# Optimization experiments

Hardware: AMD Instinct MI355X
Metric: run time of the kernel (lower is better)

The kernel has to match this reference:

```python
import jax, jax.numpy as jnp
import numpy as np
from jax import lax

B, T, I, H, O = 64, 512, 256, 1024, 1


def setup_inputs() -> dict:
    key = jax.random.key(0)
    ks = jax.random.split(key, 7)
    s_ih = 1.0 / np.sqrt(H)
    return {
        "x": jax.random.normal(ks[0], (B, T, I), dtype=jnp.float32),
        "W_ih": jax.random.uniform(ks[1], (4 * H, I), minval=-s_ih, maxval=s_ih, dtype=jnp.float32),
        "W_hh": jax.random.uniform(ks[2], (4 * H, H), minval=-s_ih, maxval=s_ih, dtype=jnp.float32),
        "b_ih": jax.random.uniform(ks[3], (4 * H,), minval=-s_ih, maxval=s_ih, dtype=jnp.float32),
        "b_hh": jax.random.uniform(ks[4], (4 * H,), minval=-s_ih, maxval=s_ih, dtype=jnp.float32),
        "fc_W": jax.random.uniform(ks[5], (O, H), minval=-s_ih, maxval=s_ih, dtype=jnp.float32),
        "fc_b": jax.random.uniform(ks[6], (O,), minval=-s_ih, maxval=s_ih, dtype=jnp.float32),
    }


def reference(x, W_ih, W_hh, b_ih, b_hh, fc_W, fc_b):
    Bd, Td, _ = x.shape
    Hd = W_hh.shape[1]
    # Precompute input projections for all timesteps: [T, B, 4H]
    x_proj = jnp.einsum('bti,gi->tbg', x, W_ih) + b_ih + b_hh

    def step(carry, xt):
        h, c = carry
        gates = xt + h @ W_hh.T  # [B, 4H]
        i_g, f_g, g_g, o_g = jnp.split(gates, 4, axis=-1)  # PyTorch order i,f,g,o
        i_g = jax.nn.sigmoid(i_g)
        f_g = jax.nn.sigmoid(f_g)
        g_g = jnp.tanh(g_g)
        o_g = jax.nn.sigmoid(o_g)
        c_new = f_g * c + i_g * g_g
        h_new = o_g * jnp.tanh(c_new)
        return (h_new, c_new), None

    h0 = jnp.zeros((Bd, Hd), dtype=x.dtype)
    c0 = jnp.zeros((Bd, Hd), dtype=x.dtype)
    (h_last, _), _ = lax.scan(step, (h0, c0), x_proj)
    out = jnp.tanh(h_last)          # tanh on last hidden state
    return out @ fc_W.T + fc_b      # [B, O]
```

## Files before the change

kernel.cpp:

```cpp
#include <hip/hip_runtime.h>
#include <hip/hip_bf16.h>


typedef __bf16 bf16_t;
typedef bf16_t b16x8 __attribute__((ext_vector_type(8)));
typedef short  s16x8 __attribute__((ext_vector_type(8)));
typedef float  f32x4 __attribute__((ext_vector_type(4)));

#define TQ 512
#define IQ 256
#define HQ 1024

union U8 { b16x8 b; s16x8 s; unsigned short u[8]; unsigned long long q[2]; };

__device__ __forceinline__ float bf2f(unsigned short s) {
    return __uint_as_float(((unsigned)s) << 16);
}
__device__ __forceinline__ unsigned short f2bf(float f) {
    unsigned u = __float_as_uint(f);
    u += 0x7fff + ((u >> 16) & 1);
    return (unsigned short)(u >> 16);
}
__device__ __forceinline__ b16x8 cvt84(float4 a, float4 b) {
    U8 r;
    r.u[0] = f2bf(a.x); r.u[1] = f2bf(a.y); r.u[2] = f2bf(a.z); r.u[3] = f2bf(a.w);
    r.u[4] = f2bf(b.x); r.u[5] = f2bf(b.y); r.u[6] = f2bf(b.z); r.u[7] = f2bf(b.w);
    return r.b;
}
__device__ __forceinline__ b16x8 load_h16(const unsigned short* p) {
    U8 r;
    r.q[0] = __hip_atomic_load((const unsigned long long*)p,
                               __ATOMIC_RELAXED, __HIP_MEMORY_SCOPE_AGENT);
    r.q[1] = __hip_atomic_load((const unsigned long long*)(p + 4),
                               __ATOMIC_RELAXED, __HIP_MEMORY_SCOPE_AGENT);
    return r.b;
}
__device__ __forceinline__ float sigm(float x) {
    return 1.f / (1.f + __expf(-x));
}
__device__ __forceinline__ float tanh_f(float v) {
    float x = fminf(fmaxf(v, -15.f), 15.f);
    float e = __expf(2.f * x);
    return (e - 1.f) / (e + 1.f);
}

__launch_bounds__(512, 2)
__global__ void lstm_persist(const float* __restrict__ x,
                             const float* __restrict__ Wih,
                             const float* __restrict__ Whh,
                             const float* __restrict__ bih,
                             const float* __restrict__ bhh,
                             const float* __restrict__ fcW,
                             const float* __restrict__ fcb,
                             float* __restrict__ out,
                             unsigned short* __restrict__ hbuf,
                             unsigned int* __restrict__ bar)
{
    __shared__ float red[8 * 4 * 64 * 4];

    const int tid  = threadIdx.x;
    const int w    = tid >> 6;
    const int lane = tid & 63;
    const int bid  = blockIdx.x;
    const int bg   = bid & 3;
    const int ug   = bid >> 2;

    const int l16  = lane & 15;
    const int quad = lane >> 4;

    b16x8 wih[4];
    b16x8 whh[4][4];
    {
        const int koff = quad * 8;
        #pragma unroll
        for (int g = 0; g < 4; ++g) {
            int row = g * HQ + ug * 16 + l16;
            const float* p = Wih + (size_t)row * IQ + w * 32 + koff;
            float4 a = *(const float4*)p;
            float4 b = *(const float4*)(p + 4);
            wih[g] = cvt84(a, b);
            #pragma unroll
            for (int j = 0; j < 4; ++j) {
                int k0 = (w * 4 + j) * 32 + koff;
                const float* q = Whh + (size_t)row * HQ + k0;
                float4 c = *(const float4*)q;
                float4 d = *(const float4*)(q + 4);
                whh[j][g] = cvt84(c, d);
            }
        }
    }

    float c_st[4] = {0.f, 0.f, 0.f, 0.f};
    float bias_r[4];
    if (w == 0) {
        #pragma unroll
        for (int g = 0; g < 4; ++g) {
            int gr = g * HQ + ug * 16 + l16;
            bias_r[g] = bih[gr] + bhh[gr];
        }
    }

    unsigned int* mybar = &bar[bg * 64];

    const float* xbase = x + ((size_t)(bg * 16 + l16) * TQ) * IQ + w * 32 + quad * 8;
    float4 xa = *(const float4*)(xbase);
    float4 xb = *(const float4*)(xbase + 4);

    for (int t = 0; t < TQ; ++t) {
        const int p = t & 1;

        b16x8 ax = cvt84(xa, xb);
        f32x4 acc[4];
        #pragma unroll
        for (int g = 0; g < 4; ++g) {
            f32x4 z = {0.f, 0.f, 0.f, 0.f};
            acc[g] = __builtin_amdgcn_mfma_f32_16x16x32_bf16(ax, wih[g], z, 0, 0, 0);
        }

        if (t && tid == 0) {
            unsigned target = 64u * (unsigned)t;
            while (__hip_atomic_load(mybar, __ATOMIC_RELAXED,
                                     __HIP_MEMORY_SCOPE_AGENT) < target)
                __builtin_amdgcn_s_sleep(1);
        }
        __syncthreads();
        asm volatile("" ::: "memory");

        const unsigned short* hread = hbuf + ((size_t)p * 4 + bg) * (16 * HQ);
        b16x8 ah[4];
        #pragma unroll
        for (int j = 0; j < 4; ++j)
            ah[j] = load_h16(hread + (size_t)l16 * HQ + (w * 4 + j) * 32 + quad * 8);
        #pragma unroll
        for (int j = 0; j < 4; ++j) {
            #pragma unroll
            for (int g = 0; g < 4; ++g)
                acc[g] = __builtin_amdgcn_mfma_f32_16x16x32_bf16(ah[j], whh[j][g], acc[g], 0, 0, 0);
        }

        #pragma unroll
        for (int g = 0; g < 4; ++g)
            *(f32x4*)&red[((w * 4 + g) * 64 + lane) * 4] = acc[g];
        __syncthreads();

        {
            size_t nt = (t + 1 < TQ) ? (size_t)(t + 1) * IQ : (size_t)t * IQ;
            xa = *(const float4*)(xbase + nt);
            xb = *(const float4*)(xbase + nt + 4);
        }

        if (w == 0) {
            f32x4 gv[4];
            #pragma unroll
            for (int g = 0; g < 4; ++g) {
                f32x4 s = *(const f32x4*)&red[((0 * 4 + g) * 64 + lane) * 4];
                #pragma unroll
                for (int ww = 1; ww < 8; ++ww)
                    s += *(const f32x4*)&red[((ww * 4 + g) * 64 + lane) * 4];
                gv[g] = s;
            }
            unsigned short* hw = hbuf + ((size_t)(p ^ 1) * 4 + bg) * (16 * HQ)
                               + (size_t)ug * 16 + l16;
            #pragma unroll
            for (int r = 0; r < 4; ++r) {
                float gi = gv[0][r] + bias_r[0];
                float gf = gv[1][r] + bias_r[1];
                float gg = gv[2][r] + bias_r[2];
                float go = gv[3][r] + bias_r[3];
                float i_s = sigm(gi);
                float f_s = sigm(gf);
                float g_t = tanh_f(gg);
                float o_s = sigm(go);
                float c = f_s * c_st[r] + i_s * g_t;
                c_st[r] = c;
                float h = o_s * tanh_f(c);
                int b = quad * 4 + r;
                __hip_atomic_store(hw + (size_t)b * HQ, f2bf(h),
                                   __ATOMIC_RELAXED, __HIP_MEMORY_SCOPE_AGENT);
            }
            __builtin_amdgcn_s_waitcnt(0);
            if (tid == 0)
                __hip_atomic_fetch_add(mybar, 1u, __ATOMIC_RELAXED,
                                       __HIP_MEMORY_SCOPE_AGENT);
        }
    }

    if (bid < 4) {
        if (tid == 0) {
            unsigned target = 64u * (unsigned)TQ;
            while (__hip_atomic_load(mybar, __ATOMIC_RELAXED,
                                     __HIP_MEMORY_SCOPE_AGENT) < target)
                __builtin_amdgcn_s_sleep(1);
        }
        __syncthreads();
        const unsigned short* hl = hbuf + (size_t)bg * (16 * HQ);
        float fb = fcb[0];
        #pragma unroll
        for (int r = 0; r < 2; ++r) {
            int b = w * 2 + r;
            float s = 0.f;
            #pragma unroll
            for (int j = 0; j < 16; ++j) {
                int u = j * 64 + lane;
                unsigned short hv = __hip_atomic_load(hl + b * HQ + u,
                                                      __ATOMIC_RELAXED,
                                                      __HIP_MEMORY_SCOPE_AGENT);
                s += tanh_f(bf2f(hv)) * fcW[u];
            }
            #pragma unroll
            for (int off = 32; off > 0; off >>= 1)
                s += __shfl_down(s, off);
            if (lane == 0) out[bg * 16 + b] = s + fb;
        }
    }
}

extern "C" void kernel_launch(void* const* d_in, const int* in_sizes, int n_in,
                              void* d_out, int out_size, void* d_ws, size_t ws_size,
                              hipStream_t stream) {
    (void)in_sizes; (void)n_in; (void)out_size; (void)ws_size;
    const float* x   = (const float*)d_in[0];
    const float* Wih = (const float*)d_in[1];
    const float* Whh = (const float*)d_in[2];
    const float* bih = (const float*)d_in[3];
    const float* bhh = (const float*)d_in[4];
    const float* fcW = (const float*)d_in[5];
    const float* fcb = (const float*)d_in[6];
    float* out = (float*)d_out;

    unsigned short* hbuf = (unsigned short*)d_ws;
    unsigned int*   bar  = (unsigned int*)((char*)d_ws + 262144);

    hipMemsetAsync(d_ws, 0, 262144 + 1024, stream);

    void* args[] = { &x, &Wih, &Whh, &bih, &bhh, &fcW, &fcb, &out, &hbuf, &bar };
    hipLaunchCooperativeKernel(reinterpret_cast<void*>(lstm_persist),
                               dim3(256), dim3(512), args, 0, stream);
}
```

Baseline: 2.462 ms.

## Replace atomic counter barrier with per-producer flags polled per wave

```diff
diff --git a/kernel.cpp b/kernel.cpp
--- a/kernel.cpp
+++ b/kernel.cpp
@@ -4,14 +4,13 @@
 
 typedef __bf16 bf16_t;
 typedef bf16_t b16x8 __attribute__((ext_vector_type(8)));
-typedef short  s16x8 __attribute__((ext_vector_type(8)));
 typedef float  f32x4 __attribute__((ext_vector_type(4)));
 
 #define TQ 512
 #define IQ 256
 #define HQ 1024
 
-union U8 { b16x8 b; s16x8 s; unsigned short u[8]; unsigned long long q[2]; };
+union U8 { b16x8 b; unsigned long long q[2]; unsigned short u[8]; };
 
 __device__ __forceinline__ float bf2f(unsigned short s) {
     return __uint_as_float(((unsigned)s) << 16);
@@ -56,7 +55,7 @@
                              unsigned short* __restrict__ hbuf,
                              unsigned int* __restrict__ bar)
 {
-    __shared__ float red[8 * 4 * 64 * 4];
+    __shared__ float red[2 * 8192];
 
     const int tid  = threadIdx.x;
     const int w    = tid >> 6;
@@ -100,7 +99,8 @@
         }
     }
 
-    unsigned int* mybar = &bar[bg * 64];
+    unsigned int* fl = bar + (size_t)bg * 1024;
+    const unsigned int* myfl = fl + (size_t)(w * 8 + (lane & 7)) * 16;
 
     const float* xbase = x + ((size_t)(bg * 16 + l16) * TQ) * IQ + w * 32 + quad * 8;
     float4 xa = *(const float4*)(xbase);
@@ -117,14 +117,14 @@
             acc[g] = __builtin_amdgcn_mfma_f32_16x16x32_bf16(ax, wih[g], z, 0, 0, 0);
         }
 
-        if (t && tid == 0) {
-            unsigned target = 64u * (unsigned)t;
-            while (__hip_atomic_load(mybar, __ATOMIC_RELAXED,
-                                     __HIP_MEMORY_SCOPE_AGENT) < target)
-                __builtin_amdgcn_s_sleep(1);
-        }
-        __syncthreads();
-        asm volatile("" ::: "memory");
+        if (t) {
+            unsigned tv = (unsigned)t;
+            unsigned v = __hip_atomic_load(myfl, __ATOMIC_RELAXED,
+                                           __HIP_MEMORY_SCOPE_AGENT);
+            while (!__all(v >= tv))
+                v = __hip_atomic_load(myfl, __ATOMIC_RELAXED,
+                                      __HIP_MEMORY_SCOPE_AGENT);
+        }
 
         const unsigned short* hread = hbuf + ((size_t)p * 4 + bg) * (16 * HQ);
         b16x8 ah[4];
@@ -138,25 +138,20 @@
                 acc[g] = __builtin_amdgcn_mfma_f32_16x16x32_bf16(ah[j], whh[j][g], acc[g], 0, 0, 0);
         }
 
+        float* rb = &red[p * 8192];
         #pragma unroll
         for (int g = 0; g < 4; ++g)
-            *(f32x4*)&red[((w * 4 + g) * 64 + lane) * 4] = acc[g];
+            *(f32x4*)&rb[((w * 4 + g) * 64 + lane) * 4] = acc[g];
         __syncthreads();
-
-        {
-            size_t nt = (t + 1 < TQ) ? (size_t)(t + 1) * IQ : (size_t)t * IQ;
-            xa = *(const float4*)(xbase + nt);
-            xb = *(const float4*)(xbase + nt + 4);
-        }
 
         if (w == 0) {
             f32x4 gv[4];
             #pragma unroll
             for (int g = 0; g < 4; ++g) {
-                f32x4 s = *(const f32x4*)&red[((0 * 4 + g) * 64 + lane) * 4];
+                f32x4 s = *(const f32x4*)&rb[((0 * 4 + g) * 64 + lane) * 4];
                 #pragma unroll
                 for (int ww = 1; ww < 8; ++ww)
-                    s += *(const f32x4*)&red[((ww * 4 + g) * 64 + lane) * 4];
+                    s += *(const f32x4*)&rb[((ww * 4 + g) * 64 + lane) * 4];
                 gv[g] = s;
             }
             unsigned short* hw = hbuf + ((size_t)(p ^ 1) * 4 + bg) * (16 * HQ)
@@ -178,19 +173,28 @@
                 __hip_atomic_store(hw + (size_t)b * HQ, f2bf(h),
                                    __ATOMIC_RELAXED, __HIP_MEMORY_SCOPE_AGENT);
             }
-            __builtin_amdgcn_s_waitcnt(0);
-            if (tid == 0)
-                __hip_atomic_fetch_add(mybar, 1u, __ATOMIC_RELAXED,
-                                       __HIP_MEMORY_SCOPE_AGENT);
+            asm volatile("s_waitcnt vmcnt(0)" ::: "memory");
+            if (lane == 0)
+                __hip_atomic_store(fl + (size_t)ug * 16, (unsigned)(t + 1),
+                                   __ATOMIC_RELAXED, __HIP_MEMORY_SCOPE_AGENT);
+            size_t nt = (t + 1 < TQ) ? (size_t)(t + 1) * IQ : (size_t)t * IQ;
+            xa = *(const float4*)(xbase + nt);
+            xb = *(const float4*)(xbase + nt + 4);
+        } else {
+            size_t nt = (t + 1 < TQ) ? (size_t)(t + 1) * IQ : (size_t)t * IQ;
+            xa = *(const float4*)(xbase + nt);
+            xb = *(const float4*)(xbase + nt + 4);
         }
     }
 
     if (bid < 4) {
-        if (tid == 0) {
-            unsigned target = 64u * (unsigned)TQ;
-            while (__hip_atomic_load(mybar, __ATOMIC_RELAXED,
-                                     __HIP_MEMORY_SCOPE_AGENT) < target)
-                __builtin_amdgcn_s_sleep(1);
+        if (w == 0) {
+            const unsigned int* pf = fl + (size_t)lane * 16;
+            unsigned v = __hip_atomic_load(pf, __ATOMIC_RELAXED,
+                                           __HIP_MEMORY_SCOPE_AGENT);
+            while (!__all(v >= (unsigned)TQ))
+                v = __hip_atomic_load(pf, __ATOMIC_RELAXED,
+                                      __HIP_MEMORY_SCOPE_AGENT);
         }
         __syncthreads();
         const unsigned short* hl = hbuf + (size_t)bg * (16 * HQ);
@@ -231,7 +235,7 @@
     unsigned short* hbuf = (unsigned short*)d_ws;
     unsigned int*   bar  = (unsigned int*)((char*)d_ws + 262144);
 
-    hipMemsetAsync(d_ws, 0, 262144 + 1024, stream);
+    hipMemsetAsync(d_ws, 0, 262144 + 16384, stream);
 
     void* args[] = { &x, &Wih, &Whh, &bih, &bhh, &fcW, &fcb, &out, &hbuf, &bar };
     hipLaunchCooperativeKernel(reinterpret_cast<void*>(lstm_persist),
```

New measurement: 2.375 ms. -3.5%, faster.
